# Optimization experiments

Measured on AMD Instinct MI355X. Metric: run time of the kernel, lower is better.

Reference implementation:

```python
import jax, jax.numpy as jnp
import numpy as np


def setup_inputs() -> dict:
    key = jax.random.key(0)
    k1, k2, k3 = jax.random.split(key, 3)
    B, N, D = 16, 512, 256
    # integer frame durations per token, 4..11 frames (avg ~7.5)
    durations = jax.random.randint(k1, (B, N), 4, 12, dtype=jnp.int32)
    # T = max over batch of total frames (static python int, mirrors torch.arange(0, max(s)))
    total_len = int(jnp.max(jnp.sum(durations, axis=-1)))
    x = jax.random.normal(k2, (B, N, D), dtype=jnp.float32)
    # positive Gaussian range (std) per token
    ranges = jax.random.uniform(k3, (B, N), minval=0.5, maxval=4.0, dtype=jnp.float32)
    return {"x": x, "durations": durations, "ranges": ranges, "total_len": total_len}


def _gaussian_weights(durations, ranges, total_len):
    # e: cumulative end frame per token, c: Gaussian center per token
    e = jnp.cumsum(durations, axis=-1).astype(jnp.float32)          # [B, N]
    c = (e - 0.5 * durations.astype(jnp.float32))[..., None]        # [B, N, 1]
    t = jnp.arange(total_len, dtype=jnp.float32)[None, None, :]     # [1, 1, T]
    inv_r2 = ranges[..., None] ** (-2)                               # [B, N, 1]
    w1 = jnp.exp(-inv_r2 * (t - c) ** 2)                             # [B, N, T]
    # original computes the exp twice (w_1 and inside w_2); same math, computed once
    w2 = jnp.sum(w1, axis=1, keepdims=True) + 1e-20                  # [B, 1, T]
    return w1 / w2


def _create_positions(durations, total_len):
    # frame-index-within-token positions: pos[b, t] = t - start_of_segment(t)
    e = jnp.cumsum(durations, axis=-1)                               # [B, N]
    starts = e - durations                                           # [B, N]
    t = jnp.arange(total_len, dtype=durations.dtype)                 # [T]
    seg = jax.vmap(lambda eb: jnp.searchsorted(eb, t, side='right'))(e)  # [B, T]
    seg = jnp.clip(seg, 0, durations.shape[-1] - 1)
    return t[None, :] - jnp.take_along_axis(starts, seg, axis=-1)    # [B, T]


def reference(x, durations, ranges, total_len):
    weights = _gaussian_weights(durations, ranges, total_len)        # [B, N, T]
    # matmul(weights.transpose(1,2), x) -> [B, T, D]
    out = jnp.einsum('bnt,bnd->btd', weights, x)
    positions = _create_positions(durations, total_len)
    return positions, out, weights
```

## Files before the change

kernel.cpp:

```cpp
#include <hip/hip_runtime.h>
#include <hip/hip_bf16.h>


#define TT  64
#define NWC 44
#define WBS 72
#define MARGIN 42.0f
#define RPB 4

typedef __attribute__((ext_vector_type(8))) short short8;
typedef __attribute__((ext_vector_type(8))) unsigned short ushort8;
typedef __attribute__((ext_vector_type(4))) float f32x4;

__device__ inline unsigned short f2bf(float f) {
    union { float f; unsigned int u; } v; v.f = f;
    unsigned int u = v.u;
    return (unsigned short)((u + 0x7FFFu + ((u >> 16) & 1u)) >> 16);
}

__global__ __launch_bounds__(256) void xpose_kernel(
        const float* __restrict__ x, unsigned short* __restrict__ xT) {
    int n0 = blockIdx.x * 64, d0 = blockIdx.y * 64, b = blockIdx.z;
    int tid = threadIdx.x;
    __shared__ unsigned short tile[64][72];
    const float* xb = x + ((size_t)b * 512 + n0) * 256 + d0;
    int dl = tid & 63, ng = tid >> 6;
    #pragma unroll
    for (int i = 0; i < 16; i++) {
        int nl = ng * 16 + i;
        tile[nl][dl] = f2bf(xb[(size_t)nl * 256 + dl]);
    }
    __syncthreads();
    unsigned short* xTb = xT + (size_t)b * 131072;
    #pragma unroll
    for (int it = 0; it < 2; it++) {
        int ci  = it * 256 + tid;
        int l15 = ci & 15;
        int sub = ci >> 4;
        int tkb = sub & 7, dkb = sub >> 3;
        ushort8 v;
        #pragma unroll
        for (int k = 0; k < 8; k++) v[k] = tile[tkb * 8 + k][dkb * 16 + l15];
        *(ushort8*)(xTb + ((((blockIdx.y * 4 + dkb) * 64) + blockIdx.x * 8 + tkb) << 7)
                        + (l15 << 3)) = v;
    }
}

__global__ __launch_bounds__(512) void scan_kernel(
        const int* __restrict__ dur, const float* __restrict__ ranges,
        float* __restrict__ c, float* __restrict__ ir,
        int* __restrict__ e_i, int* __restrict__ st_i) {
    const int N = 512;
    int b = blockIdx.x, tid = threadIdx.x;
    int lane = tid & 63, wid = tid >> 6;
    int d = dur[b * N + tid];
    int v = d;
    #pragma unroll
    for (int off = 1; off < 64; off <<= 1) {
        int t = __shfl_up(v, off);
        if (lane >= off) v += t;
    }
    __shared__ int wsum[8], woff[8];
    if (lane == 63) wsum[wid] = v;
    __syncthreads();
    if (tid == 0) { int a = 0; for (int i = 0; i < 8; i++) { woff[i] = a; a += wsum[i]; } }
    __syncthreads();
    int e = v + woff[wid];
    float r = ranges[b * N + tid];
    c[b * N + tid]    = (float)e - 0.5f * (float)d;
    ir[b * N + tid]   = 1.0f / (r * r);
    e_i[b * N + tid]  = e;
    st_i[b * N + tid] = e - d;
}

__global__ __launch_bounds__(256) void pass1_kernel(
        const unsigned short* __restrict__ xT, const float* __restrict__ c,
        const float* __restrict__ ir,
        const int* __restrict__ e_i, const int* __restrict__ st_i,
        float* __restrict__ pos_out ,
        float* __restrict__ out1 ,
        float* __restrict__ iw2_ws ,
        int T) {
    const int N = 512;
    const int D = 256;
    int b = blockIdx.y;
    int t0 = blockIdx.x * TT;
    int tid = threadIdx.x;

    __shared__ float c_s[512];
    __shared__ float ir_s[512];
    __shared__ int   es[512], ss[512];
    __shared__ __align__(16) unsigned short wb[TT][WBS];
    __shared__ float part[4][TT];
    __shared__ float iw2_s[TT];
    __shared__ int lohi[2];

    for (int i = tid; i < 512; i += 256) {
        c_s[i]  = c[b * N + i];
        ir_s[i] = ir[b * N + i];
        es[i]   = e_i[b * N + i];
        ss[i]   = st_i[b * N + i];
    }
    __syncthreads();

    if (tid == 0) {
        float lo_v = (float)t0 - MARGIN;
        float hi_v = (float)(t0 + TT - 1) + MARGIN;
        int lo = 0, hi = 512;
        while (lo < hi) { int m = (lo + hi) >> 1; if (c_s[m] < lo_v) lo = m + 1; else hi = m; }
        int l = lo;
        lo = 0; hi = 512;
        while (lo < hi) { int m = (lo + hi) >> 1; if (c_s[m] <= hi_v) lo = m + 1; else hi = m; }
        int h = lo - 1;
        if (h > l + NWC - 1) h = l + NWC - 1;
        l &= ~7;
        if (l > 448) l = 448;
        lohi[0] = l; lohi[1] = h;
    }
    if (tid < TT) {
        int t = t0 + tid;
        if (t < T) {
            int lo = 0, hi = 512;
            while (lo < hi) { int m = (lo + hi) >> 1; if (es[m] <= t) lo = m + 1; else hi = m; }
            int seg = min(lo, 511);
            pos_out[b * T + t] = (float)(t - ss[seg]);
        }
    }
    __syncthreads();
    int lo_u = lohi[0], hi_u = lohi[1];

    int tl = tid & 63;
    int s  = tid >> 6;
    int t  = t0 + tl;

    ushort8 wv0, wv1;
    float p = 0.f;
    #pragma unroll
    for (int jj = 0; jj < 16; jj++) {
        int n = lo_u + 16 * s + jj;
        float w1 = 0.f;
        if (n <= hi_u && t < T) {
            float dd = (float)t - c_s[n];
            w1 = expf(-ir_s[n] * dd * dd);
        }
        unsigned short hb = f2bf(w1);
        if (jj < 8) wv0[jj] = hb; else wv1[jj - 8] = hb;
        p += w1;
    }
    *(ushort8*)&wb[tl][16 * s]     = wv0;
    *(ushort8*)&wb[tl][16 * s + 8] = wv1;
    part[s][tl] = p;
    __syncthreads();
    if (tid < TT) {
        float w2 = part[0][tid] + part[1][tid] + part[2][tid] + part[3][tid];
        float iw2 = 1.0f / (w2 + 1e-20f);
        iw2_s[tid] = iw2;
        int t2 = t0 + tid;
        if (t2 < T) iw2_ws[b * T + t2] = iw2;
    }
    __syncthreads();

    int lane = tid & 63;
    int l15  = lane & 15;
    int q    = lane >> 4;

    f32x4 acc[4][4];
    #pragma unroll
    for (int mt = 0; mt < 4; mt++)
        #pragma unroll
        for (int nt = 0; nt < 4; nt++)
            acc[mt][nt] = (f32x4){0.f, 0.f, 0.f, 0.f};

    const unsigned short* xTb = xT + (size_t)b * 131072;
    #pragma unroll
    for (int ks = 0; ks < 2; ks++) {
        int tokb = (lo_u >> 3) + ks * 4 + q;
        short8 afrag[4];
        #pragma unroll
        for (int mt = 0; mt < 4; mt++)
            afrag[mt] = *(const short8*)&wb[16 * mt + l15][ks * 32 + q * 8];
        #pragma unroll
        for (int nt = 0; nt < 4; nt++) {
            int dblk = 4 * s + nt;
            short8 bfrag = *(const short8*)(xTb + (((dblk << 6) + tokb) << 7) + (l15 << 3));
            #pragma unroll
            for (int mt = 0; mt < 4; mt++)
                acc[mt][nt] = __builtin_amdgcn_mfma_f32_16x16x32_bf16(afrag[mt], bfrag, acc[mt][nt], 0, 0, 0);
        }
    }

    #pragma unroll
    for (int mt = 0; mt < 4; mt++) {
        #pragma unroll
        for (int r = 0; r < 4; r++) {
            int tt = t0 + 16 * mt + q * 4 + r;
            if (tt < T) {
                float iw2 = iw2_s[16 * mt + q * 4 + r];
                float* orow = out1 + ((size_t)b * T + tt) * D + 64 * s;
                #pragma unroll
                for (int nt = 0; nt < 4; nt++)
                    orow[nt * 16 + l15] = acc[mt][nt][r] * iw2;
            }
        }
    }
}

__global__ __launch_bounds__(256) void weights_kernel(
        const float* __restrict__ c, const float* __restrict__ ir,
        const float* __restrict__ iw2_ws,
        float* __restrict__ out2 , int T) {
    const int N = 512;
    int b = blockIdx.y;
    int n0 = blockIdx.x * RPB;
    int tid = threadIdx.x;
    const f32x4 z4 = (f32x4){0.f, 0.f, 0.f, 0.f};

    for (int r = 0; r < RPB; r++) {
        int n = n0 + r;
        float cn  = c[b * N + n];
        float irn = ir[b * N + n];
        float rad = 10.3f * __frsqrt_rn(irn) + 1.0f;
        int lo = (int)(cn - rad); if (lo < 0) lo = 0;
        int hi = (int)(cn + rad) + 1; if (hi > T) hi = T;

        size_t base = ((size_t)b * N + n) * (size_t)T;
        int head = (int)((4 - (base & 3)) & 3);
        if (head > T) head = T;
        if (tid < head) {
            int t = tid;
            float w = 0.f;
            if (t >= lo && t < hi) {
                float d = (float)t - cn;
                w = expf(-irn * d * d) * iw2_ws[b * T + t];
            }
            out2[base + t] = w;
        }
        int ngrp = (T - head) >> 2;
        int tail = (T - head) & 3;
        float* rowp = (float*)(out2 + base + head);
        for (int g = tid; g < ngrp; g += 256) {
            int tg = head + 4 * g;
            f32x4 v = z4;
            if (tg + 3 >= lo && tg < hi) {
                #pragma unroll
                for (int k = 0; k < 4; k++) {
                    int t = tg + k;
                    if (t >= lo && t < hi) {
                        float d = (float)t - cn;
                        v[k] = expf(-irn * d * d) * iw2_ws[b * T + t];
                    }
                }
            }
            *(f32x4*)(rowp + 4 * g) = v;
        }
        if (tid < tail) {
            int t = head + 4 * ngrp + tid;
            float w = 0.f;
            if (t >= lo && t < hi) {
                float d = (float)t - cn;
                w = expf(-irn * d * d) * iw2_ws[b * T + t];
            }
            out2[base + t] = w;
        }
    }
}

extern "C" void kernel_launch(void* const* d_in, const int* in_sizes, int n_in,
                              void* d_out, int out_size, void* d_ws, size_t ws_size,
                              hipStream_t stream) {
    const float* x      = (const float*)d_in[0];
    const int*   dur    = (const int*)d_in[1];
    const float* ranges = (const float*)d_in[2];
    const int B = 16, N = 512, D = 256;
    const int T = out_size / (B * (1 + D + N));

    float* pos_out = (float*)d_out;
    float* out1    = pos_out + (size_t)B * T;
    float* out2    = out1 + (size_t)B * T * D;

    float* c      = (float*)d_ws;
    float* ir     = c + B * N;
    int*   e_i    = (int*)(ir + B * N);
    int*   st_i   = e_i + B * N;
    float* iw2_ws = (float*)(st_i + B * N);
    size_t xoff   = 4 * (size_t)(B * N) + (size_t)B * T;
    xoff = (xoff + 7) & ~(size_t)7;
    unsigned short* xT = (unsigned short*)((float*)d_ws + xoff);

    xpose_kernel<<<dim3(8, 4, B), 256, 0, stream>>>(x, xT);

    scan_kernel<<<B, 512, 0, stream>>>(dur, ranges, c, ir, e_i, st_i);

    dim3 g1((T + TT - 1) / TT, B);
    pass1_kernel<<<g1, 256, 0, stream>>>(xT, c, ir, e_i, st_i, pos_out, out1, iw2_ws, T);

    dim3 g2(N / RPB, B);
    weights_kernel<<<g2, 256, 0, stream>>>(c, ir, iw2_ws, out2, T);
}
```

Before: 220.8 us.

## Fuse scan, transpose and weight zero-fill into one kernel; write weights in pass1

Merges the scan and bf16 transpose kernels into one launch that also zero-fills the whole weights output in bulk with vector stores. The separate weights kernel is removed. pass1 now writes the nonzero band of normalized weights directly from its shared iw2 values, so the iw2 workspace round trip and the exp recomputation there go away. The trade-offs are a full zero pass over the large weights tensor followed by scattered, strided scalar band writes from pass1 (one per token row per t). Correctness also depends on the pass1 band covering every value that is not negligibly small.

```diff
diff --git a/kernel.cpp b/kernel.cpp
--- a/kernel.cpp
+++ b/kernel.cpp
@@ -6,7 +6,10 @@
 #define NWC 44
 #define WBS 72
 #define MARGIN 42.0f
-#define RPB 4
+
+#define SCB 16
+#define XPB 512
+#define ZFB 2048
 
 typedef __attribute__((ext_vector_type(8))) short short8;
 typedef __attribute__((ext_vector_type(8))) unsigned short ushort8;
@@ -18,59 +21,69 @@
     return (unsigned short)((u + 0x7FFFu + ((u >> 16) & 1u)) >> 16);
 }
 
-__global__ __launch_bounds__(256) void xpose_kernel(
-        const float* __restrict__ x, unsigned short* __restrict__ xT) {
-    int n0 = blockIdx.x * 64, d0 = blockIdx.y * 64, b = blockIdx.z;
-    int tid = threadIdx.x;
+__global__ __launch_bounds__(512) void k1_combo(
+        const float* __restrict__ x, const int* __restrict__ dur,
+        const float* __restrict__ ranges,
+        unsigned short* __restrict__ xT,
+        float* __restrict__ c, float* __restrict__ ir,
+        int* __restrict__ e_i, int* __restrict__ st_i,
+        float* __restrict__ out2, int T) {
+    const int N = 512;
+    int bid = blockIdx.x, tid = threadIdx.x;
+
     __shared__ unsigned short tile[64][72];
-    const float* xb = x + ((size_t)b * 512 + n0) * 256 + d0;
-    int dl = tid & 63, ng = tid >> 6;
-    #pragma unroll
-    for (int i = 0; i < 16; i++) {
-        int nl = ng * 16 + i;
-        tile[nl][dl] = f2bf(xb[(size_t)nl * 256 + dl]);
-    }
-    __syncthreads();
-    unsigned short* xTb = xT + (size_t)b * 131072;
-    #pragma unroll
-    for (int it = 0; it < 2; it++) {
-        int ci  = it * 256 + tid;
+    __shared__ int wsum[8], woff[8];
+
+    if (bid < SCB) {
+        int b = bid;
+        int lane = tid & 63, wid = tid >> 6;
+        int d = dur[b * N + tid];
+        int v = d;
+        #pragma unroll
+        for (int off = 1; off < 64; off <<= 1) {
+            int t = __shfl_up(v, off);
+            if (lane >= off) v += t;
+        }
+        if (lane == 63) wsum[wid] = v;
+        __syncthreads();
+        if (tid == 0) { int a = 0; for (int i = 0; i < 8; i++) { woff[i] = a; a += wsum[i]; } }
+        __syncthreads();
+        int e = v + woff[wid];
+        float r = ranges[b * N + tid];
+        c[b * N + tid]    = (float)e - 0.5f * (float)d;
+        ir[b * N + tid]   = 1.0f / (r * r);
+        e_i[b * N + tid]  = e;
+        st_i[b * N + tid] = e - d;
+    } else if (bid < SCB + XPB) {
+        int v = bid - SCB;
+        int bx = v & 7, by = (v >> 3) & 3, b = v >> 5;
+        int n0 = bx * 64, d0 = by * 64;
+        const float* xb = x + ((size_t)b * 512 + n0) * 256 + d0;
+        int dl = tid & 63, ng = tid >> 6;
+        #pragma unroll
+        for (int i = 0; i < 8; i++) {
+            int nl = ng * 8 + i;
+            tile[nl][dl] = f2bf(xb[(size_t)nl * 256 + dl]);
+        }
+        __syncthreads();
+        unsigned short* xTb = xT + (size_t)b * 131072;
+        int ci  = tid;
         int l15 = ci & 15;
         int sub = ci >> 4;
         int tkb = sub & 7, dkb = sub >> 3;
-        ushort8 v;
-        #pragma unroll
-        for (int k = 0; k < 8; k++) v[k] = tile[tkb * 8 + k][dkb * 16 + l15];
-        *(ushort8*)(xTb + ((((blockIdx.y * 4 + dkb) * 64) + blockIdx.x * 8 + tkb) << 7)
-                        + (l15 << 3)) = v;
-    }
-}
-
-__global__ __launch_bounds__(512) void scan_kernel(
-        const int* __restrict__ dur, const float* __restrict__ ranges,
-        float* __restrict__ c, float* __restrict__ ir,
-        int* __restrict__ e_i, int* __restrict__ st_i) {
-    const int N = 512;
-    int b = blockIdx.x, tid = threadIdx.x;
-    int lane = tid & 63, wid = tid >> 6;
-    int d = dur[b * N + tid];
-    int v = d;
-    #pragma unroll
-    for (int off = 1; off < 64; off <<= 1) {
-        int t = __shfl_up(v, off);
-        if (lane >= off) v += t;
-    }
-    __shared__ int wsum[8], woff[8];
-    if (lane == 63) wsum[wid] = v;
-    __syncthreads();
-    if (tid == 0) { int a = 0; for (int i = 0; i < 8; i++) { woff[i] = a; a += wsum[i]; } }
-    __syncthreads();
-    int e = v + woff[wid];
-    float r = ranges[b * N + tid];
-    c[b * N + tid]    = (float)e - 0.5f * (float)d;
-    ir[b * N + tid]   = 1.0f / (r * r);
-    e_i[b * N + tid]  = e;
-    st_i[b * N + tid] = e - d;
+        ushort8 vv;
+        #pragma unroll
+        for (int k = 0; k < 8; k++) vv[k] = tile[tkb * 8 + k][dkb * 16 + l15];
+        *(ushort8*)(xTb + ((((by * 4 + dkb) * 64) + bx * 8 + tkb) << 7)
+                        + (l15 << 3)) = vv;
+    } else {
+        const f32x4 z4 = (f32x4){0.f, 0.f, 0.f, 0.f};
+        f32x4* p = (f32x4*)out2;
+        size_t nv4 = (size_t)2048 * (size_t)T;
+        size_t stride = (size_t)ZFB * 512;
+        for (size_t i = (size_t)(bid - SCB - XPB) * 512 + tid; i < nv4; i += stride)
+            p[i] = z4;
+    }
 }
 
 __global__ __launch_bounds__(256) void pass1_kernel(
@@ -79,7 +92,7 @@
         const int* __restrict__ e_i, const int* __restrict__ st_i,
         float* __restrict__ pos_out ,
         float* __restrict__ out1 ,
-        float* __restrict__ iw2_ws ,
+        float* __restrict__ out2 ,
         int T) {
     const int N = 512;
     const int D = 256;
@@ -153,10 +166,7 @@
     __syncthreads();
     if (tid < TT) {
         float w2 = part[0][tid] + part[1][tid] + part[2][tid] + part[3][tid];
-        float iw2 = 1.0f / (w2 + 1e-20f);
-        iw2_s[tid] = iw2;
-        int t2 = t0 + tid;
-        if (t2 < T) iw2_ws[b * T + t2] = iw2;
+        iw2_s[tid] = 1.0f / (w2 + 1e-20f);
     }
     __syncthreads();
 
@@ -203,64 +213,15 @@
             }
         }
     }
-}
-
-__global__ __launch_bounds__(256) void weights_kernel(
-        const float* __restrict__ c, const float* __restrict__ ir,
-        const float* __restrict__ iw2_ws,
-        float* __restrict__ out2 , int T) {
-    const int N = 512;
-    int b = blockIdx.y;
-    int n0 = blockIdx.x * RPB;
-    int tid = threadIdx.x;
-    const f32x4 z4 = (f32x4){0.f, 0.f, 0.f, 0.f};
-
-    for (int r = 0; r < RPB; r++) {
-        int n = n0 + r;
-        float cn  = c[b * N + n];
-        float irn = ir[b * N + n];
-        float rad = 10.3f * __frsqrt_rn(irn) + 1.0f;
-        int lo = (int)(cn - rad); if (lo < 0) lo = 0;
-        int hi = (int)(cn + rad) + 1; if (hi > T) hi = T;
-
-        size_t base = ((size_t)b * N + n) * (size_t)T;
-        int head = (int)((4 - (base & 3)) & 3);
-        if (head > T) head = T;
-        if (tid < head) {
-            int t = tid;
-            float w = 0.f;
-            if (t >= lo && t < hi) {
-                float d = (float)t - cn;
-                w = expf(-irn * d * d) * iw2_ws[b * T + t];
-            }
-            out2[base + t] = w;
-        }
-        int ngrp = (T - head) >> 2;
-        int tail = (T - head) & 3;
-        float* rowp = (float*)(out2 + base + head);
-        for (int g = tid; g < ngrp; g += 256) {
-            int tg = head + 4 * g;
-            f32x4 v = z4;
-            if (tg + 3 >= lo && tg < hi) {
-                #pragma unroll
-                for (int k = 0; k < 4; k++) {
-                    int t = tg + k;
-                    if (t >= lo && t < hi) {
-                        float d = (float)t - cn;
-                        v[k] = expf(-irn * d * d) * iw2_ws[b * T + t];
-                    }
-                }
-            }
-            *(f32x4*)(rowp + 4 * g) = v;
-        }
-        if (tid < tail) {
-            int t = head + 4 * ngrp + tid;
-            float w = 0.f;
-            if (t >= lo && t < hi) {
-                float d = (float)t - cn;
-                w = expf(-irn * d * d) * iw2_ws[b * T + t];
-            }
-            out2[base + t] = w;
+
+    if (t < T) {
+        float iw2l = iw2_s[tl];
+        int nw = hi_u - lo_u + 1;
+        for (int i = s; i < nw; i += 4) {
+            int n = lo_u + i;
+            float dd = (float)t - c_s[n];
+            float w = expf(-ir_s[n] * dd * dd) * iw2l;
+            out2[((size_t)b * N + n) * (size_t)T + t] = w;
         }
     }
 }
@@ -282,18 +243,12 @@
     float* ir     = c + B * N;
     int*   e_i    = (int*)(ir + B * N);
     int*   st_i   = e_i + B * N;
-    float* iw2_ws = (float*)(st_i + B * N);
-    size_t xoff   = 4 * (size_t)(B * N) + (size_t)B * T;
-    xoff = (xoff + 7) & ~(size_t)7;
-    unsigned short* xT = (unsigned short*)((float*)d_ws + xoff);
-
-    xpose_kernel<<<dim3(8, 4, B), 256, 0, stream>>>(x, xT);
-
-    scan_kernel<<<B, 512, 0, stream>>>(dur, ranges, c, ir, e_i, st_i);
+    unsigned short* xT = (unsigned short*)(st_i + B * N);
+
+    k1_combo<<<SCB + XPB + ZFB, 512, 0, stream>>>(x, dur, ranges, xT,
+                                                  c, ir, e_i, st_i, out2, T);
 
     dim3 g1((T + TT - 1) / TT, B);
-    pass1_kernel<<<g1, 256, 0, stream>>>(xT, c, ir, e_i, st_i, pos_out, out1, iw2_ws, T);
-
-    dim3 g2(N / RPB, B);
-    weights_kernel<<<g2, 256, 0, stream>>>(c, ir, iw2_ws, out2, T);
-}
+    pass1_kernel<<<g1, 256, 0, stream>>>(xT, c, ir, e_i, st_i,
+                                         pos_out, out1, out2, T);
+}
```

Measured after the change: 211.6 us. 1.04x faster.
